# Performance work log

Hardware: AMD Instinct MI355X
Metric: run time of the kernel (lower is better)

The kernel has to match this reference:

```python
import jax, jax.numpy as jnp
import numpy as np

N = 50000          # num nodes
E = 800000         # num edges
H, C = 2, 64       # heads, per-head channels (hidden_dim=64)
IN_DIM = 128
EDGE_DIM = 32
NEG_SLOPE = 0.2


def setup_inputs() -> dict:
    key = jax.random.key(0)
    ks = jax.random.split(key, 20)
    s = 0.05
    inp = {
        'x': jax.random.normal(ks[0], (N, IN_DIM), jnp.float32),
        'edge_index': jax.random.randint(ks[1], (2, E), 0, N, jnp.int64),
        'edge_attr': jax.random.normal(ks[2], (E, EDGE_DIM), jnp.float32),
    }
    k = 3
    for l in range(3):
        inp[f'Wl{l}'] = jax.random.normal(ks[k], (IN_DIM, H * C), jnp.float32) * s; k += 1
        inp[f'Wr{l}'] = jax.random.normal(ks[k], (IN_DIM, H * C), jnp.float32) * s; k += 1
        inp[f'We{l}'] = jax.random.normal(ks[k], (EDGE_DIM, H * C), jnp.float32) * s; k += 1
        inp[f'att{l}'] = jax.random.normal(ks[k], (H, C), jnp.float32) * s; k += 1
        inp[f'b{l}'] = jnp.zeros((H * C,), jnp.float32)
    return inp


def gatv2_layer(x, src, dst, edge_attr, Wl, Wr, We, att, b):
    # PyG GATv2Conv (concat=True, share_weights=False):
    #   e_ij = att . LeakyReLU(Wl x_j + Wr x_i + We edge_ij)
    #   alpha = softmax_j over neighborhood of dst i; out_i = sum_j alpha_ij * (Wl x_j)
    xl = (x @ Wl).reshape(-1, H, C)              # [N,H,C] source transform
    xr = (x @ Wr).reshape(-1, H, C)              # [N,H,C] target transform
    ea = (edge_attr @ We).reshape(-1, H, C)      # [E,H,C]
    xj = xl[src]                                 # [E,H,C] gather source
    e = jax.nn.leaky_relu(xj + xr[dst] + ea, NEG_SLOPE)
    logits = jnp.einsum('ehc,hc->eh', e, att)    # [E,H]
    # segment softmax over dst neighborhoods
    m = jax.ops.segment_max(logits, dst, num_segments=N)  # [N,H]
    m = jnp.where(jnp.isfinite(m), m, 0.0)
    ex = jnp.exp(logits - m[dst])
    denom = jax.ops.segment_sum(ex, dst, num_segments=N)  # [N,H]
    alpha = ex / (denom[dst] + 1e-16)            # [E,H]
    out = jax.ops.segment_sum(alpha[:, :, None] * xj, dst, num_segments=N)  # [N,H,C]
    return out.reshape(-1, H * C) + b


def reference(x, edge_index, edge_attr,
              Wl0, Wr0, We0, att0, b0,
              Wl1, Wr1, We1, att1, b1,
              Wl2, Wr2, We2, att2, b2):
    src, dst = edge_index[0], edge_index[1]
    h = gatv2_layer(x, src, dst, edge_attr, Wl0, Wr0, We0, att0, b0)
    h = jax.nn.relu(h)
    h = gatv2_layer(h, src, dst, edge_attr, Wl1, Wr1, We1, att1, b1)
    h = jax.nn.relu(h)
    h = gatv2_layer(h, src, dst, edge_attr, Wl2, Wr2, We2, att2, b2)
    return h
```

## Files before the change

kernel.cpp:

```cpp
#include <hip/hip_runtime.h>

typedef unsigned int u32;
typedef unsigned short u16;
typedef __attribute__((ext_vector_type(8))) short bf16x8;
typedef __attribute__((ext_vector_type(4))) float f32x4;

__device__ __forceinline__ u16 f2b(float f){
  u32 x = __float_as_uint(f);
  u32 r = (x + 0x7fffu + ((x >> 16) & 1u)) >> 16;
  return (u16)r;
}
__device__ __forceinline__ float b2f(u16 h){ return __uint_as_float((u32)h << 16); }
__device__ __forceinline__ float bl(u32 u){ return __uint_as_float(u << 16); }
__device__ __forceinline__ float bh(u32 u){ return __uint_as_float(u & 0xffff0000u); }


__global__ void k_detect(const u32* __restrict__ ei, int n, u32* __restrict__ flag){
  int t = blockIdx.x * blockDim.x + threadIdx.x;
  u32 v = 0;
  if (t < n) v = ei[2 * t + 1];
  unsigned long long b = __ballot(v != 0u);
  if ((threadIdx.x & 63) == 0 && b) atomicOr(flag, 1u);
}

__global__ void k_convhist(const int* __restrict__ ei, int* __restrict__ src, int* __restrict__ dst,
                           int* __restrict__ deg, const float* __restrict__ eattr,
                           u16* __restrict__ ea2, int E, const u32* __restrict__ flag){
  int e = blockIdx.x * blockDim.x + threadIdx.x;
  if (e >= E) return;
  bool is64 = (*flag == 0u);
  int s, d;
  if (is64){ s = ei[2 * e]; d = ei[2 * (E + e)]; }
  else     { s = ei[e];     d = ei[E + e]; }
  src[e] = s; dst[e] = d;
  atomicAdd(&deg[d], 1);
  const float4* srow = (const float4*)(eattr + (size_t)e * 32);
  u32 pk[16];
  #pragma unroll
  for (int i = 0; i < 8; i++){
    float4 v = srow[i];
    pk[2*i]   = (u32)f2b(v.x) | ((u32)f2b(v.y) << 16);
    pk[2*i+1] = (u32)f2b(v.z) | ((u32)f2b(v.w) << 16);
  }
  uint4* drow = (uint4*)(ea2 + (size_t)e * 32);
  drow[0] = make_uint4(pk[0], pk[1], pk[2], pk[3]);
  drow[1] = make_uint4(pk[4], pk[5], pk[6], pk[7]);
  drow[2] = make_uint4(pk[8], pk[9], pk[10], pk[11]);
  drow[3] = make_uint4(pk[12], pk[13], pk[14], pk[15]);
}

__global__ __launch_bounds__(256) void k_scan1(const int* __restrict__ deg, int* __restrict__ bsum, int n){
  int b = blockIdx.x, t = threadIdx.x, lane = t & 63, wv = t >> 6;
  int i0 = b * 1024 + t * 4;
  int4 v = make_int4(0,0,0,0);
  if (i0 + 3 < n) v = *(const int4*)(deg + i0);
  else { if (i0 < n) v.x = deg[i0]; if (i0+1 < n) v.y = deg[i0+1]; if (i0+2 < n) v.z = deg[i0+2]; }
  int s = v.x + v.y + v.z + v.w;
  #pragma unroll
  for (int off = 1; off < 64; off <<= 1) s += __shfl_xor(s, off);
  __shared__ int ws[4];
  if (lane == 0) ws[wv] = s;
  __syncthreads();
  if (t == 0) bsum[b] = ws[0] + ws[1] + ws[2] + ws[3];
}

__global__ __launch_bounds__(1024) void k_scan2(int* __restrict__ bsum, int nb, int* __restrict__ segN){
  int t = threadIdx.x, lane = t & 63, w = t >> 6;
  int v = (t < nb) ? bsum[t] : 0;
  int x = v;
  #pragma unroll
  for (int off = 1; off < 64; off <<= 1){
    int y = __shfl_up(x, off);
    if (lane >= off) x += y;
  }
  __shared__ int wsum[16];
  if (lane == 63) wsum[w] = x;
  __syncthreads();
  if (w == 0 && lane < 16){
    int sv = wsum[lane];
    #pragma unroll
    for (int off = 1; off < 16; off <<= 1){
      int y = __shfl_up(sv, off);
      if (lane >= off) sv += y;
    }
    wsum[lane] = sv;
  }
  __syncthreads();
  int woff = (w > 0) ? wsum[w - 1] : 0;
  if (t < nb) bsum[t] = woff + x - v;
  if (t == 0) *segN = wsum[15];
}

__global__ __launch_bounds__(256) void k_scan3(const int* __restrict__ deg, const int* __restrict__ bsum,
                                               int* __restrict__ seg, int n){
  int b = blockIdx.x, t = threadIdx.x, lane = t & 63, wv = t >> 6;
  int i0 = b * 1024 + t * 4;
  int4 v = make_int4(0,0,0,0);
  if (i0 + 3 < n) v = *(const int4*)(deg + i0);
  else { if (i0 < n) v.x = deg[i0]; if (i0+1 < n) v.y = deg[i0+1]; if (i0+2 < n) v.z = deg[i0+2]; }
  int s = v.x + v.y + v.z + v.w;
  int x = s;
  #pragma unroll
  for (int off = 1; off < 64; off <<= 1){
    int y = __shfl_up(x, off);
    if (lane >= off) x += y;
  }
  __shared__ int ws[4];
  if (lane == 63) ws[wv] = x;
  __syncthreads();
  int woff = 0;
  #pragma unroll
  for (int k = 0; k < 4; k++) if (k < wv) woff += ws[k];
  int base = bsum[b] + woff + (x - s);
  if (i0 < n)     seg[i0]     = base;
  if (i0+1 < n)   seg[i0+1]   = base + v.x;
  if (i0+2 < n)   seg[i0+2]   = base + v.x + v.y;
  if (i0+3 < n)   seg[i0+3]   = base + v.x + v.y + v.z;
}

__global__ void k_scatter(const int* __restrict__ src, const int* __restrict__ dst,
                          const int* __restrict__ seg, int* __restrict__ cur,
                          int* __restrict__ ssrc, int* __restrict__ sdst,
                          int* __restrict__ seid, int E){
  int e = blockIdx.x * blockDim.x + threadIdx.x;
  if (e >= E) return;
  int d = dst[e];
  int pos = seg[d] + atomicAdd(&cur[d], 1);
  ssrc[pos] = src[e];
  sdst[pos] = d;
  seid[pos] = e;
}

__global__ void k_sortb(const int* __restrict__ seid, const u16* __restrict__ ea2o,
                        u16* __restrict__ ea2s, int E){
  int t = blockIdx.x * blockDim.x + threadIdx.x;
  int e = t >> 2, j = t & 3;
  if (e >= E) return;
  int eid = seid[e];
  uint4 v = *(const uint4*)(ea2o + (size_t)eid * 32 + j * 8);
  *(uint4*)(ea2s + (size_t)e * 32 + j * 8) = v;
}

__global__ __launch_bounds__(256) void k_prepw(
    const float* __restrict__ W0, const float* __restrict__ W1, const float* __restrict__ W2,
    const float* __restrict__ W3, const float* __restrict__ W4, const float* __restrict__ W5,
    u16* __restrict__ WtH, u16* __restrict__ WtL)
{
  int mat = blockIdx.z;
  const float* W = (mat == 0) ? W0 : (mat == 1) ? W1 : (mat == 2) ? W2 :
                   (mat == 3) ? W3 : (mat == 4) ? W4 : W5;
  __shared__ float tile[32][33];
  int kt = blockIdx.x * 32, ct = blockIdx.y * 32;
  int tr = threadIdx.x & 31, ti = threadIdx.x >> 5;
  #pragma unroll
  for (int j = 0; j < 4; j++){
    int kk = ti + 8 * j;
    tile[kk][tr] = W[(size_t)(kt + kk) * 128 + ct + tr];
  }
  __syncthreads();
  #pragma unroll
  for (int j = 0; j < 4; j++){
    int cc = ti + 8 * j;
    float v = tile[tr][cc];
    u16 hi = f2b(v);
    u16 lo = f2b(v - b2f(hi));
    size_t o = (size_t)mat * 16384 + (size_t)(ct + cc) * 128 + kt + tr;
    WtH[o] = hi;
    WtL[o] = lo;
  }
}

__global__ __launch_bounds__(256) void k_gemm2(
    const float* __restrict__ A,
    const u16* __restrict__ WtH, const u16* __restrict__ WtL,
    u16* __restrict__ xlb, u16* __restrict__ xrb, int nrows)
{
  __shared__ u16 sAH[64][72], sAL[64][72];
  __shared__ u16 sWH[128][72], sWL[128][72];
  int t = threadIdx.x, wv = t >> 6, lane = t & 63;
  int col = lane & 15, kg = lane >> 4;
  int r0 = blockIdx.x * 64;
  int mat = blockIdx.y;
  const u16* WHb = WtH + (size_t)mat * 16384;
  const u16* WLb = WtL + (size_t)mat * 16384;

  f32x4 acc[4][2];
  #pragma unroll
  for (int m = 0; m < 4; m++)
    #pragma unroll
    for (int n = 0; n < 2; n++)
      acc[m][n] = (f32x4){0.f, 0.f, 0.f, 0.f};

  int ar = t >> 2, ak = (t & 3) << 4;
  int wc = t >> 1, wk = (t & 1) << 5;

  for (int kh = 0; kh < 2; kh++){
    __syncthreads();
    {
      int gr = r0 + ar;
      const float* ap = A + (size_t)gr * 128 + kh * 64 + ak;
      float4 va = {0,0,0,0}, vb = {0,0,0,0}, vc = {0,0,0,0}, vd = {0,0,0,0};
      if (gr < nrows){
        va = *(const float4*)ap; vb = *(const float4*)(ap + 4);
        vc = *(const float4*)(ap + 8); vd = *(const float4*)(ap + 12);
      }
      float fv[16] = { va.x, va.y, va.z, va.w, vb.x, vb.y, vb.z, vb.w,
                       vc.x, vc.y, vc.z, vc.w, vd.x, vd.y, vd.z, vd.w };
      u32 hp[8], lp[8];
      #pragma unroll
      for (int i = 0; i < 8; i++){
        u16 h0 = f2b(fv[2*i]),   h1 = f2b(fv[2*i+1]);
        u16 l0 = f2b(fv[2*i]   - b2f(h0));
        u16 l1 = f2b(fv[2*i+1] - b2f(h1));
        hp[i] = (u32)h0 | ((u32)h1 << 16);
        lp[i] = (u32)l0 | ((u32)l1 << 16);
      }
      *(uint4*)&sAH[ar][ak]     = make_uint4(hp[0], hp[1], hp[2], hp[3]);
      *(uint4*)&sAH[ar][ak + 8] = make_uint4(hp[4], hp[5], hp[6], hp[7]);
      *(uint4*)&sAL[ar][ak]     = make_uint4(lp[0], lp[1], lp[2], lp[3]);
      *(uint4*)&sAL[ar][ak + 8] = make_uint4(lp[4], lp[5], lp[6], lp[7]);
    }
    {
      const u16* gh = WHb + (size_t)wc * 128 + kh * 64 + wk;
      const u16* gl = WLb + (size_t)wc * 128 + kh * 64 + wk;
      uint4 h0 = *(const uint4*)gh, h1 = *(const uint4*)(gh + 8);
      uint4 h2 = *(const uint4*)(gh + 16), h3 = *(const uint4*)(gh + 24);
      uint4 l0 = *(const uint4*)gl, l1 = *(const uint4*)(gl + 8);
      uint4 l2 = *(const uint4*)(gl + 16), l3 = *(const uint4*)(gl + 24);
      *(uint4*)&sWH[wc][wk]      = h0; *(uint4*)&sWH[wc][wk + 8]  = h1;
      *(uint4*)&sWH[wc][wk + 16] = h2; *(uint4*)&sWH[wc][wk + 24] = h3;
      *(uint4*)&sWL[wc][wk]      = l0; *(uint4*)&sWL[wc][wk + 8]  = l1;
      *(uint4*)&sWL[wc][wk + 16] = l2; *(uint4*)&sWL[wc][wk + 24] = l3;
    }
    __syncthreads();
    #pragma unroll
    for (int ks = 0; ks < 2; ks++){
      bf16x8 bhi0 = *(const bf16x8*)&sWH[wv*32 + col]     [ks*32 + kg*8];
      bf16x8 bhi1 = *(const bf16x8*)&sWH[wv*32 + 16 + col][ks*32 + kg*8];
      bf16x8 blo0 = *(const bf16x8*)&sWL[wv*32 + col]     [ks*32 + kg*8];
      bf16x8 blo1 = *(const bf16x8*)&sWL[wv*32 + 16 + col][ks*32 + kg*8];
      #pragma unroll
      for (int m = 0; m < 4; m++){
        bf16x8 ahv = *(const bf16x8*)&sAH[m*16 + col][ks*32 + kg*8];
        bf16x8 alv = *(const bf16x8*)&sAL[m*16 + col][ks*32 + kg*8];
        acc[m][0] = __builtin_amdgcn_mfma_f32_16x16x32_bf16(ahv, bhi0, acc[m][0], 0, 0, 0);
        acc[m][0] = __builtin_amdgcn_mfma_f32_16x16x32_bf16(alv, bhi0, acc[m][0], 0, 0, 0);
        acc[m][0] = __builtin_amdgcn_mfma_f32_16x16x32_bf16(ahv, blo0, acc[m][0], 0, 0, 0);
        acc[m][1] = __builtin_amdgcn_mfma_f32_16x16x32_bf16(ahv, bhi1, acc[m][1], 0, 0, 0);
        acc[m][1] = __builtin_amdgcn_mfma_f32_16x16x32_bf16(alv, bhi1, acc[m][1], 0, 0, 0);
        acc[m][1] = __builtin_amdgcn_mfma_f32_16x16x32_bf16(ahv, blo1, acc[m][1], 0, 0, 0);
      }
    }
  }
  u16* ob = mat ? xrb : xlb;
  #pragma unroll
  for (int m = 0; m < 4; m++){
    #pragma unroll
    for (int n = 0; n < 2; n++){
      #pragma unroll
      for (int r = 0; r < 4; r++){
        int row = r0 + m*16 + kg*4 + r;
        int c   = wv*32 + n*16 + col;
        if (row < nrows) ob[(size_t)row * 128 + c] = f2b(acc[m][n][r]);
      }
    }
  }
}

__global__ __launch_bounds__(256) void k_edge(
    const int* __restrict__ ssrc, const int* __restrict__ sdst,
    const u16* __restrict__ ea2s,
    const u16* __restrict__ xlb, const u16* __restrict__ xrb,
    const float* __restrict__ We, const float* __restrict__ att,
    float2* __restrict__ pr2, int ntiles, int E)
{
  __shared__ float sD[4][16][132];
  int wv = threadIdx.x >> 6, lane = threadIdx.x & 63;
  int col = lane & 15, kg = lane >> 4;
  int er = lane >> 2, q = lane & 3;

  bf16x8 bw[8];
  #pragma unroll
  for (int c = 0; c < 8; c++)
    #pragma unroll
    for (int j = 0; j < 8; j++)
      bw[c][j] = (short)f2b(We[(kg * 8 + j) * 128 + c * 16 + col]);
  u32 attp[16];
  #pragma unroll
  for (int i = 0; i < 16; i++)
    attp[i] = (u32)f2b(att[q * 32 + 2*i]) | ((u32)f2b(att[q * 32 + 2*i + 1]) << 16);

  int nw = gridDim.x * 4;
  int t = blockIdx.x * 4 + wv;
  if (t >= ntiles) return;

  int e0 = t * 16;
  bf16x8 a = *(const bf16x8*)(ea2s + (size_t)(e0 + col) * 32 + kg * 8);
  int p = e0 + er;
  int sn = ssrc[p], dn = sdst[p];
  const u16* xjp = xlb + (size_t)sn * 128 + q * 32;
  const u16* xip = xrb + (size_t)dn * 128 + q * 32;
  uint4 j0 = ((const uint4*)xjp)[0], j1 = ((const uint4*)xjp)[1],
        j2 = ((const uint4*)xjp)[2], j3 = ((const uint4*)xjp)[3];
  uint4 i0 = ((const uint4*)xip)[0], i1 = ((const uint4*)xip)[1],
        i2 = ((const uint4*)xip)[2], i3 = ((const uint4*)xip)[3];

  while (true){
    int t2 = t + nw;
    bool more = (t2 < ntiles);
    int tc = more ? t2 : t;
    int e02 = tc * 16;
    int p2 = e02 + er;
    int sn2 = ssrc[p2], dn2 = sdst[p2];
    bf16x8 a2 = *(const bf16x8*)(ea2s + (size_t)(e02 + col) * 32 + kg * 8);

    #pragma unroll
    for (int c = 0; c < 8; c++){
      f32x4 d = __builtin_amdgcn_mfma_f32_16x16x32_bf16(a, bw[c], (f32x4){0.f,0.f,0.f,0.f}, 0, 0, 0);
      #pragma unroll
      for (int r = 0; r < 4; r++)
        sD[wv][kg * 4 + r][c * 16 + col] = d[r];
    }

    const u16* xj2 = xlb + (size_t)sn2 * 128 + q * 32;
    const u16* xi2 = xrb + (size_t)dn2 * 128 + q * 32;
    uint4 nj0 = ((const uint4*)xj2)[0], nj1 = ((const uint4*)xj2)[1],
          nj2 = ((const uint4*)xj2)[2], nj3 = ((const uint4*)xj2)[3];
    uint4 ni0 = ((const uint4*)xi2)[0], ni1 = ((const uint4*)xi2)[1],
          ni2 = ((const uint4*)xi2)[2], ni3 = ((const uint4*)xi2)[3];

    const float* drow = &sD[wv][er][q * 32];
    float acc = 0.f;
#define EPK(KO, JQ, IQ) { \
    float4 d0 = *(const float4*)(drow + KO*8); \
    float4 d1 = *(const float4*)(drow + KO*8 + 4); \
    float v; u32 jw, iw, aw; \
    jw = JQ.x; iw = IQ.x; aw = attp[KO*4+0]; \
    v = d0.x + bl(jw) + bl(iw); v = fmaxf(v, 0.2f*v); acc = fmaf(v, bl(aw), acc); \
    v = d0.y + bh(jw) + bh(iw); v = fmaxf(v, 0.2f*v); acc = fmaf(v, bh(aw), acc); \
    jw = JQ.y; iw = IQ.y; aw = attp[KO*4+1]; \
    v = d0.z + bl(jw) + bl(iw); v = fmaxf(v, 0.2f*v); acc = fmaf(v, bl(aw), acc); \
    v = d0.w + bh(jw) + bh(iw); v = fmaxf(v, 0.2f*v); acc = fmaf(v, bh(aw), acc); \
    jw = JQ.z; iw = IQ.z; aw = attp[KO*4+2]; \
    v = d1.x + bl(jw) + bl(iw); v = fmaxf(v, 0.2f*v); acc = fmaf(v, bl(aw), acc); \
    v = d1.y + bh(jw) + bh(iw); v = fmaxf(v, 0.2f*v); acc = fmaf(v, bh(aw), acc); \
    jw = JQ.w; iw = IQ.w; aw = attp[KO*4+3]; \
    v = d1.z + bl(jw) + bl(iw); v = fmaxf(v, 0.2f*v); acc = fmaf(v, bl(aw), acc); \
    v = d1.w + bh(jw) + bh(iw); v = fmaxf(v, 0.2f*v); acc = fmaf(v, bh(aw), acc); }
    EPK(0, j0, i0) EPK(1, j1, i1) EPK(2, j2, i2) EPK(3, j3, i3)
#undef EPK
    acc += __shfl_xor(acc, 1);
    float other = __shfl_xor(acc, 2);
    if (q == 0 && p < E){
      pr2[p] = make_float2(__expf(fminf(acc, 80.f)), __expf(fminf(other, 80.f)));
    }
    if (!more) break;
    t = t2; p = p2; a = a2;
    j0 = nj0; j1 = nj1; j2 = nj2; j3 = nj3;
    i0 = ni0; i1 = ni1; i2 = ni2; i3 = ni3;
  }
}

template<int RELU>
__global__ __launch_bounds__(256) void k_seg2(
    const int* __restrict__ seg, const int* __restrict__ ssrc,
    const float2* __restrict__ pr2,
    const u16* __restrict__ xlb, const float* __restrict__ bias,
    float* __restrict__ out, int N)
{
  int wid  = blockIdx.x * 4 + (threadIdx.x >> 6);
  int lane = threadIdx.x & 63;
  if (wid >= N) return;
  int c0 = lane * 2, head = lane >> 5;

  int p0 = seg[wid], p1 = seg[wid + 1];
  float2 bv = *(const float2*)(bias + c0);
  float s = 0.f, o0 = 0.f, o1 = 0.f;

  if (p0 < p1){
#define LDB(K, PP, QN, XN) \
    { int ii = (PP + K < p1) ? (PP + K) : (p1 - 1); \
      int ss = ssrc[ii]; \
      QN = pr2[ii]; \
      XN = *(const u32*)(xlb + (size_t)ss * 128 + c0); }
    float2 qa0, qa1, qa2, qa3, qa4, qa5, qa6, qa7;
    u32 xa0, xa1, xa2, xa3, xa4, xa5, xa6, xa7;
    LDB(0, p0, qa0, xa0) LDB(1, p0, qa1, xa1) LDB(2, p0, qa2, xa2) LDB(3, p0, qa3, xa3)
    LDB(4, p0, qa4, xa4) LDB(5, p0, qa5, xa5) LDB(6, p0, qa6, xa6) LDB(7, p0, qa7, xa7)
    int p = p0;
    while (true){
      int pn = p + 8;
      bool more = pn < p1;
      int pc = more ? pn : p;
      float2 qb0, qb1, qb2, qb3, qb4, qb5, qb6, qb7;
      u32 xb0, xb1, xb2, xb3, xb4, xb5, xb6, xb7;
      LDB(0, pc, qb0, xb0) LDB(1, pc, qb1, xb1) LDB(2, pc, qb2, xb2) LDB(3, pc, qb3, xb3)
      LDB(4, pc, qb4, xb4) LDB(5, pc, qb5, xb5) LDB(6, pc, qb6, xb6) LDB(7, pc, qb7, xb7)
#define ACC(K, QN, XN) { \
      float e = head ? QN.y : QN.x; \
      if (p + K >= p1) e = 0.f; \
      s += e; \
      o0 = fmaf(e, bl(XN), o0); \
      o1 = fmaf(e, bh(XN), o1); }
      ACC(0, qa0, xa0) ACC(1, qa1, xa1) ACC(2, qa2, xa2) ACC(3, qa3, xa3)
      ACC(4, qa4, xa4) ACC(5, qa5, xa5) ACC(6, qa6, xa6) ACC(7, qa7, xa7)
#undef ACC
      if (!more) break;
      p = pn;
      qa0 = qb0; xa0 = xb0; qa1 = qb1; xa1 = xb1;
      qa2 = qb2; xa2 = xb2; qa3 = qb3; xa3 = xb3;
      qa4 = qb4; xa4 = xb4; qa5 = qb5; xa5 = xb5;
      qa6 = qb6; xa6 = xb6; qa7 = qb7; xa7 = xb7;
    }
#undef LDB
  }
  float inv = 1.0f / (s + 1e-16f);
  float r0 = fmaf(o0, inv, bv.x);
  float r1 = fmaf(o1, inv, bv.y);
  if (RELU){ r0 = fmaxf(r0, 0.f); r1 = fmaxf(r1, 0.f); }
  *(float2*)(out + (size_t)wid * 128 + c0) = make_float2(r0, r1);
}

extern "C" void kernel_launch(void* const* d_in, const int* in_sizes, int n_in,
                              void* d_out, int out_size, void* d_ws, size_t ws_size,
                              hipStream_t stream)
{
  const float* x     = (const float*)d_in[0];
  const int*   ei    = (const int*)  d_in[1];
  const float* eattr = (const float*)d_in[2];
  const float* Wp[3][5];
  for (int l = 0; l < 3; l++)
    for (int j = 0; j < 5; j++)
      Wp[l][j] = (const float*)d_in[3 + l * 5 + j];

  int N = in_sizes[0] / 128;
  int E = in_sizes[2] / 32;

  char* w = (char*)d_ws;
  auto alloc = [&](size_t bytes) -> char* {
    char* p = w; w += (bytes + 255) & ~(size_t)255; return p;
  };
  float* xr   = (float*)alloc((size_t)N * 128 * 4);
  u16*   xlb  = (u16*)  alloc((size_t)N * 128 * 2);
  u16*   xrb  = (u16*)  alloc((size_t)N * 128 * 2);
  u16*   ea2o = (u16*)  alloc((size_t)E * 32 * 2);
  u16*   ea2s = (u16*)  alloc((size_t)(E + 64) * 32 * 2);
  float2* prb = (float2*)alloc((size_t)E * 8);
  u16*   WtH  = (u16*)  alloc((size_t)6 * 16384 * 2);
  u16*   WtL  = (u16*)  alloc((size_t)6 * 16384 * 2);
  int* srcA   = (int*)alloc((size_t)E * 4);
  int* dstA   = (int*)alloc((size_t)E * 4);
  int* ssrc   = (int*)alloc((size_t)(E + 64) * 4);
  int* sdst   = (int*)alloc((size_t)(E + 64) * 4);
  int* seid   = (int*)alloc((size_t)E * 4);
  int* deg    = (int*)alloc((size_t)N * 4);
  int* cur    = (int*)alloc((size_t)N * 4);
  int* seg    = (int*)alloc((size_t)(N + 1) * 4);
  int* bsum   = (int*)alloc(1024 * 4);
  u32* flag   = (u32*)alloc(256);

  hipMemsetAsync(deg,  0, (size_t)N * 4, stream);
  hipMemsetAsync(cur,  0, (size_t)N * 4, stream);
  hipMemsetAsync(flag, 0, 4, stream);
  hipMemsetAsync(ssrc + E, 0, 64 * 4, stream);
  hipMemsetAsync(sdst + E, 0, 64 * 4, stream);
  hipMemsetAsync(ea2s + (size_t)E * 32, 0, 64 * 32 * 2, stream);

  int ndet = (E < 16384) ? E : 16384;
  k_detect<<<(ndet + 255) / 256, 256, 0, stream>>>((const u32*)ei, ndet, flag);
  int gE = (E + 255) / 256;
  k_convhist<<<gE, 256, 0, stream>>>(ei, srcA, dstA, deg, eattr, ea2o, E, flag);
  int nb = (N + 1023) / 1024;
  k_scan1<<<nb, 256, 0, stream>>>(deg, bsum, N);
  k_scan2<<<1, 1024, 0, stream>>>(bsum, nb, seg + N);
  k_scan3<<<nb, 256, 0, stream>>>(deg, bsum, seg, N);
  k_scatter<<<gE, 256, 0, stream>>>(srcA, dstA, seg, cur, ssrc, sdst, seid, E);
  k_sortb<<<(E * 4 + 255) / 256, 256, 0, stream>>>(seid, ea2o, ea2s, E);
  dim3 gp(4, 4, 6);
  k_prepw<<<gp, 256, 0, stream>>>(Wp[0][0], Wp[0][1], Wp[1][0], Wp[1][1], Wp[2][0], Wp[2][1], WtH, WtL);

  int gS = (N + 3) / 4;
  int ntiles = (E + 15) / 16;
  int gEdge = (ntiles + 3) / 4; if (gEdge > 2048) gEdge = 2048;
  dim3 gG2((N + 63) / 64, 2);

  const float* hin = x;
  for (int l = 0; l < 3; l++){
    k_gemm2<<<gG2, 256, 0, stream>>>(hin, WtH + (size_t)l * 2 * 16384, WtL + (size_t)l * 2 * 16384, xlb, xrb, N);
    k_edge<<<gEdge, 256, 0, stream>>>(ssrc, sdst, ea2s, xlb, xrb, Wp[l][2], Wp[l][3], prb, ntiles, E);
    float* outp = (l == 2) ? (float*)d_out : xr;
    if (l == 2) k_seg2<0><<<gS, 256, 0, stream>>>(seg, ssrc, prb, xlb, Wp[l][4], outp, N);
    else        k_seg2<1><<<gS, 256, 0, stream>>>(seg, ssrc, prb, xlb, Wp[l][4], outp, N);
    hin = xr;
  }
}
```

Baseline: 547.7 us.

## Merge setup memsets, reschedule edge gathers, and vectorize segment aggregation

Three changes are bundled. The six setup memsets collapse into one contiguous memset, and the pad zeroing moves into k_scan1. In k_edge the xr gather is no longer prefetched a tile ahead; it is loaded at the start of each iteration, while the xl prefetch is issued before the MFMA stage, which lowers register pressure but exposes xr load latency. In k_seg2 each wave now processes 4 edges at once with 16 lanes per edge, each lane loading 8 bf16 channels as a uint4, then combines the partial sums with cross-lane shuffles, giving wider gathers and fewer loop iterations for low-degree nodes.

```diff
diff --git a/kernel.cpp b/kernel.cpp
--- a/kernel.cpp
+++ b/kernel.cpp
@@ -49,8 +49,14 @@
   drow[3] = make_uint4(pk[12], pk[13], pk[14], pk[15]);
 }
 
-__global__ __launch_bounds__(256) void k_scan1(const int* __restrict__ deg, int* __restrict__ bsum, int n){
+__global__ __launch_bounds__(256) void k_scan1(const int* __restrict__ deg, int* __restrict__ bsum, int n,
+                                               int* __restrict__ ssrc, int* __restrict__ sdst,
+                                               u16* __restrict__ ea2s_pad, int E){
   int b = blockIdx.x, t = threadIdx.x, lane = t & 63, wv = t >> 6;
+  if (b == 0){
+    if (t < 64){ ssrc[E + t] = 0; sdst[E + t] = 0; }
+    ((uint4*)ea2s_pad)[t] = make_uint4(0, 0, 0, 0);
+  }
   int i0 = b * 1024 + t * 4;
   int4 v = make_int4(0,0,0,0);
   if (i0 + 3 < n) v = *(const int4*)(deg + i0);
@@ -299,13 +305,14 @@
   int p = e0 + er;
   int sn = ssrc[p], dn = sdst[p];
   const u16* xjp = xlb + (size_t)sn * 128 + q * 32;
-  const u16* xip = xrb + (size_t)dn * 128 + q * 32;
   uint4 j0 = ((const uint4*)xjp)[0], j1 = ((const uint4*)xjp)[1],
         j2 = ((const uint4*)xjp)[2], j3 = ((const uint4*)xjp)[3];
-  uint4 i0 = ((const uint4*)xip)[0], i1 = ((const uint4*)xip)[1],
-        i2 = ((const uint4*)xip)[2], i3 = ((const uint4*)xip)[3];
 
   while (true){
+    const u16* xip = xrb + (size_t)dn * 128 + q * 32;
+    uint4 i0 = ((const uint4*)xip)[0], i1 = ((const uint4*)xip)[1],
+          i2 = ((const uint4*)xip)[2], i3 = ((const uint4*)xip)[3];
+
     int t2 = t + nw;
     bool more = (t2 < ntiles);
     int tc = more ? t2 : t;
@@ -313,6 +320,9 @@
     int p2 = e02 + er;
     int sn2 = ssrc[p2], dn2 = sdst[p2];
     bf16x8 a2 = *(const bf16x8*)(ea2s + (size_t)(e02 + col) * 32 + kg * 8);
+    const u16* xj2 = xlb + (size_t)sn2 * 128 + q * 32;
+    uint4 nj0 = ((const uint4*)xj2)[0], nj1 = ((const uint4*)xj2)[1],
+          nj2 = ((const uint4*)xj2)[2], nj3 = ((const uint4*)xj2)[3];
 
     #pragma unroll
     for (int c = 0; c < 8; c++){
@@ -321,13 +331,6 @@
       for (int r = 0; r < 4; r++)
         sD[wv][kg * 4 + r][c * 16 + col] = d[r];
     }
-
-    const u16* xj2 = xlb + (size_t)sn2 * 128 + q * 32;
-    const u16* xi2 = xrb + (size_t)dn2 * 128 + q * 32;
-    uint4 nj0 = ((const uint4*)xj2)[0], nj1 = ((const uint4*)xj2)[1],
-          nj2 = ((const uint4*)xj2)[2], nj3 = ((const uint4*)xj2)[3];
-    uint4 ni0 = ((const uint4*)xi2)[0], ni1 = ((const uint4*)xi2)[1],
-          ni2 = ((const uint4*)xi2)[2], ni3 = ((const uint4*)xi2)[3];
 
     const float* drow = &sD[wv][er][q * 32];
     float acc = 0.f;
@@ -355,9 +358,8 @@
       pr2[p] = make_float2(__expf(fminf(acc, 80.f)), __expf(fminf(other, 80.f)));
     }
     if (!more) break;
-    t = t2; p = p2; a = a2;
+    t = t2; p = p2; dn = dn2; a = a2;
     j0 = nj0; j1 = nj1; j2 = nj2; j3 = nj3;
-    i0 = ni0; i1 = ni1; i2 = ni2; i3 = ni3;
   }
 }
 
@@ -371,54 +373,65 @@
   int wid  = blockIdx.x * 4 + (threadIdx.x >> 6);
   int lane = threadIdx.x & 63;
   if (wid >= N) return;
-  int c0 = lane * 2, head = lane >> 5;
+  int eg = lane >> 4, cb = lane & 15, c0 = cb * 8;
+  int hsel = cb >> 3;
 
   int p0 = seg[wid], p1 = seg[wid + 1];
-  float2 bv = *(const float2*)(bias + c0);
-  float s = 0.f, o0 = 0.f, o1 = 0.f;
+  float s = 0.f;
+  float o0 = 0.f, o1 = 0.f, o2 = 0.f, o3 = 0.f, o4 = 0.f, o5 = 0.f, o6 = 0.f, o7 = 0.f;
 
   if (p0 < p1){
-#define LDB(K, PP, QN, XN) \
-    { int ii = (PP + K < p1) ? (PP + K) : (p1 - 1); \
-      int ss = ssrc[ii]; \
-      QN = pr2[ii]; \
-      XN = *(const u32*)(xlb + (size_t)ss * 128 + c0); }
-    float2 qa0, qa1, qa2, qa3, qa4, qa5, qa6, qa7;
-    u32 xa0, xa1, xa2, xa3, xa4, xa5, xa6, xa7;
-    LDB(0, p0, qa0, xa0) LDB(1, p0, qa1, xa1) LDB(2, p0, qa2, xa2) LDB(3, p0, qa3, xa3)
-    LDB(4, p0, qa4, xa4) LDB(5, p0, qa5, xa5) LDB(6, p0, qa6, xa6) LDB(7, p0, qa7, xa7)
+#define LDB(PP, QV, XV) { \
+    int ii = PP + eg; ii = (ii < p1) ? ii : (p1 - 1); \
+    int sn = ssrc[ii]; \
+    QV = pr2[ii]; \
+    XV = *(const uint4*)(xlb + (size_t)sn * 128 + c0); }
+    float2 qa; uint4 xa;
+    LDB(p0, qa, xa)
     int p = p0;
     while (true){
-      int pn = p + 8;
+      int pn = p + 4;
       bool more = pn < p1;
       int pc = more ? pn : p;
-      float2 qb0, qb1, qb2, qb3, qb4, qb5, qb6, qb7;
-      u32 xb0, xb1, xb2, xb3, xb4, xb5, xb6, xb7;
-      LDB(0, pc, qb0, xb0) LDB(1, pc, qb1, xb1) LDB(2, pc, qb2, xb2) LDB(3, pc, qb3, xb3)
-      LDB(4, pc, qb4, xb4) LDB(5, pc, qb5, xb5) LDB(6, pc, qb6, xb6) LDB(7, pc, qb7, xb7)
-#define ACC(K, QN, XN) { \
-      float e = head ? QN.y : QN.x; \
-      if (p + K >= p1) e = 0.f; \
-      s += e; \
-      o0 = fmaf(e, bl(XN), o0); \
-      o1 = fmaf(e, bh(XN), o1); }
-      ACC(0, qa0, xa0) ACC(1, qa1, xa1) ACC(2, qa2, xa2) ACC(3, qa3, xa3)
-      ACC(4, qa4, xa4) ACC(5, qa5, xa5) ACC(6, qa6, xa6) ACC(7, qa7, xa7)
-#undef ACC
+      float2 qb; uint4 xb;
+      LDB(pc, qb, xb)
+      float e = hsel ? qa.y : qa.x;
+      if (p + eg >= p1) e = 0.f;
+      s += e;
+      o0 = fmaf(e, bl(xa.x), o0); o1 = fmaf(e, bh(xa.x), o1);
+      o2 = fmaf(e, bl(xa.y), o2); o3 = fmaf(e, bh(xa.y), o3);
+      o4 = fmaf(e, bl(xa.z), o4); o5 = fmaf(e, bh(xa.z), o5);
+      o6 = fmaf(e, bl(xa.w), o6); o7 = fmaf(e, bh(xa.w), o7);
       if (!more) break;
-      p = pn;
-      qa0 = qb0; xa0 = xb0; qa1 = qb1; xa1 = xb1;
-      qa2 = qb2; xa2 = xb2; qa3 = qb3; xa3 = xb3;
-      qa4 = qb4; xa4 = xb4; qa5 = qb5; xa5 = xb5;
-      qa6 = qb6; xa6 = xb6; qa7 = qb7; xa7 = xb7;
+      p = pn; qa = qb; xa = xb;
     }
 #undef LDB
   }
-  float inv = 1.0f / (s + 1e-16f);
-  float r0 = fmaf(o0, inv, bv.x);
-  float r1 = fmaf(o1, inv, bv.y);
-  if (RELU){ r0 = fmaxf(r0, 0.f); r1 = fmaxf(r1, 0.f); }
-  *(float2*)(out + (size_t)wid * 128 + c0) = make_float2(r0, r1);
+  s  += __shfl_xor(s, 16);  s  += __shfl_xor(s, 32);
+  o0 += __shfl_xor(o0, 16); o0 += __shfl_xor(o0, 32);
+  o1 += __shfl_xor(o1, 16); o1 += __shfl_xor(o1, 32);
+  o2 += __shfl_xor(o2, 16); o2 += __shfl_xor(o2, 32);
+  o3 += __shfl_xor(o3, 16); o3 += __shfl_xor(o3, 32);
+  o4 += __shfl_xor(o4, 16); o4 += __shfl_xor(o4, 32);
+  o5 += __shfl_xor(o5, 16); o5 += __shfl_xor(o5, 32);
+  o6 += __shfl_xor(o6, 16); o6 += __shfl_xor(o6, 32);
+  o7 += __shfl_xor(o7, 16); o7 += __shfl_xor(o7, 32);
+
+  if (eg == 0){
+    float inv = 1.0f / (s + 1e-16f);
+    float4 b0 = *(const float4*)(bias + c0);
+    float4 b1 = *(const float4*)(bias + c0 + 4);
+    float r0 = fmaf(o0, inv, b0.x), r1 = fmaf(o1, inv, b0.y);
+    float r2 = fmaf(o2, inv, b0.z), r3 = fmaf(o3, inv, b0.w);
+    float r4 = fmaf(o4, inv, b1.x), r5 = fmaf(o5, inv, b1.y);
+    float r6 = fmaf(o6, inv, b1.z), r7 = fmaf(o7, inv, b1.w);
+    if (RELU){
+      r0 = fmaxf(r0, 0.f); r1 = fmaxf(r1, 0.f); r2 = fmaxf(r2, 0.f); r3 = fmaxf(r3, 0.f);
+      r4 = fmaxf(r4, 0.f); r5 = fmaxf(r5, 0.f); r6 = fmaxf(r6, 0.f); r7 = fmaxf(r7, 0.f);
+    }
+    *(float4*)(out + (size_t)wid * 128 + c0)     = make_float4(r0, r1, r2, r3);
+    *(float4*)(out + (size_t)wid * 128 + c0 + 4) = make_float4(r4, r5, r6, r7);
+  }
 }
 
 extern "C" void kernel_launch(void* const* d_in, const int* in_sizes, int n_in,
@@ -453,25 +466,21 @@
   int* ssrc   = (int*)alloc((size_t)(E + 64) * 4);
   int* sdst   = (int*)alloc((size_t)(E + 64) * 4);
   int* seid   = (int*)alloc((size_t)E * 4);
-  int* deg    = (int*)alloc((size_t)N * 4);
-  int* cur    = (int*)alloc((size_t)N * 4);
   int* seg    = (int*)alloc((size_t)(N + 1) * 4);
   int* bsum   = (int*)alloc(1024 * 4);
-  u32* flag   = (u32*)alloc(256);
-
-  hipMemsetAsync(deg,  0, (size_t)N * 4, stream);
-  hipMemsetAsync(cur,  0, (size_t)N * 4, stream);
-  hipMemsetAsync(flag, 0, 4, stream);
-  hipMemsetAsync(ssrc + E, 0, 64 * 4, stream);
-  hipMemsetAsync(sdst + E, 0, 64 * 4, stream);
-  hipMemsetAsync(ea2s + (size_t)E * 32, 0, 64 * 32 * 2, stream);
+  char* zbase = alloc((size_t)N * 4);      int* deg  = (int*)zbase;
+  char* zcur  = alloc((size_t)N * 4);      int* cur  = (int*)zcur;
+  char* zflag = alloc(256);                u32* flag = (u32*)zflag;
+  size_t zspan = (size_t)(zflag + 256 - zbase);
+
+  hipMemsetAsync(zbase, 0, zspan, stream);
 
   int ndet = (E < 16384) ? E : 16384;
   k_detect<<<(ndet + 255) / 256, 256, 0, stream>>>((const u32*)ei, ndet, flag);
   int gE = (E + 255) / 256;
   k_convhist<<<gE, 256, 0, stream>>>(ei, srcA, dstA, deg, eattr, ea2o, E, flag);
   int nb = (N + 1023) / 1024;
-  k_scan1<<<nb, 256, 0, stream>>>(deg, bsum, N);
+  k_scan1<<<nb, 256, 0, stream>>>(deg, bsum, N, ssrc, sdst, ea2s + (size_t)E * 32, E);
   k_scan2<<<1, 1024, 0, stream>>>(bsum, nb, seg + N);
   k_scan3<<<nb, 256, 0, stream>>>(deg, bsum, seg, N);
   k_scatter<<<gE, 256, 0, stream>>>(srcA, dstA, seg, cur, ssrc, sdst, seid, E);
```

Measured after the change: 489.8 us. 10.6% less time.
